# Kernel tuning notes

Hardware: AMD Instinct MI355X
Metric: run time of the kernel (lower is better)

Reference implementation:

```python
import jax, jax.numpy as jnp
import numpy as np

T, H, I, E, K, L, R = 1024, 2048, 1024, 16, 2, 4, 16


def setup_inputs() -> dict:
    key = jax.random.key(0)
    ks = jax.random.split(key, 10)
    hidden_states = jax.random.normal(ks[0], (T, H), jnp.float32)
    topk_ids = jax.random.randint(ks[1], (T, K), 0, E, dtype=jnp.int32)
    topk_weights = jax.random.uniform(ks[2], (T, K), jnp.float32)
    lora_indices = jax.random.randint(ks[3], (T,), 0, L, dtype=jnp.int32)
    lora_ranks = jax.random.randint(ks[4], (L,), 1, R + 1, dtype=jnp.int32)
    scalings = jax.random.uniform(ks[5], (L,), jnp.float32) + 0.5
    w1 = jax.random.normal(ks[6], (E, 2 * I, H), jnp.float32) * 0.02  # fused gate+up
    w2 = jax.random.normal(ks[7], (E, H, I), jnp.float32) * 0.02      # down proj
    lora_a = jax.random.normal(ks[8], (L, E, R, H), jnp.float32) * 0.02
    lora_b = jax.random.normal(ks[9], (L, E, H, R), jnp.float32) * 0.02
    return dict(hidden_states=hidden_states, topk_ids=topk_ids, topk_weights=topk_weights,
                lora_indices=lora_indices, lora_ranks=lora_ranks, scalings=scalings,
                w1=w1, w2=w2, lora_a=lora_a, lora_b=lora_b)


def reference(hidden_states, topk_ids, topk_weights, lora_indices, lora_ranks, scalings,
              w1, w2, lora_a, lora_b):
    x = hidden_states  # [T, H]
    # ---- Base FusedMoE (SiLU-gated), dense over all experts then routed ----
    h1 = jnp.einsum('th,efh->tef', x, w1)                 # [T, E, 2I]
    gate, up = jnp.split(h1, 2, axis=-1)                  # [T, E, I] each
    act = jax.nn.silu(gate) * up                          # [T, E, I]
    expert_out = jnp.einsum('tei,ehi->teh', act, w2)      # [T, E, H]
    route = jnp.zeros((T, E), x.dtype).at[jnp.arange(T)[:, None], topk_ids].add(topk_weights)
    base = jnp.einsum('te,teh->th', route, expert_out)    # [T, H]
    # ---- Per-expert LoRA delta (moe_dispatch + grouped LoRA GEMM) ----
    l_pair = jnp.broadcast_to(lora_indices[:, None], (T, K)).reshape(-1)  # [P], P=T*K
    e_pair = topk_ids.reshape(-1)                                         # [P]
    valid = l_pair >= 0
    l_safe = jnp.maximum(l_pair, 0)
    flat_idx = l_safe * E + e_pair                                        # index into [L*E, ...]
    A = jnp.take(lora_a.reshape(L * E, R, H), flat_idx, axis=0)           # [P, R, H]
    B = jnp.take(lora_b.reshape(L * E, H, R), flat_idx, axis=0)           # [P, H, R]
    xp = jnp.repeat(x, K, axis=0)                                         # [P, H]
    a = jnp.einsum('ph,prh->pr', xp, A)                                   # [P, R]
    ranks = jnp.maximum(lora_ranks, 1)
    rmask = jnp.arange(R)[None, :] < ranks[l_safe][:, None]               # variable rank mask
    a = jnp.where(rmask, a, 0.0) * scalings[l_safe][:, None]
    delta = jnp.einsum('pr,phr->ph', a, B)                                # [P, H]
    delta = jnp.where(valid[:, None], delta, 0.0)
    delta = delta.reshape(T, K, H).sum(axis=1)                            # merge (token,k) pairs
    return base + delta
```

## Files before the change

### kernel.cpp

```cpp
#include <hip/hip_runtime.h>
#include <math.h>

constexpr int T = 1024;
constexpr int H = 2048;
constexpr int I = 1024;
constexpr int E = 16;
constexpr int K = 2;
constexpr int L = 4;
constexpr int R = 16;
constexpr int P = T * K;
constexpr int MT_MAX = 48;
constexpr int G_CVT = T * H / (256 * 8);
constexpr int G1 = MT_MAX * 32;
constexpr int G2 = MT_MAX * 64;

typedef __attribute__((ext_vector_type(8))) short bf16x8;
typedef __attribute__((ext_vector_type(4))) float f32x4;

__device__ inline unsigned short f2bf(float f) {
  unsigned u = __builtin_bit_cast(unsigned, f);
  u = (u + 0x7FFFu + ((u >> 16) & 1u)) >> 16;
  return (unsigned short)u;
}

__device__ inline bf16x8 pack8(f32x4 a, f32x4 b) {
  bf16x8 v;
  v[0] = (short)f2bf(a[0]); v[1] = (short)f2bf(a[1]);
  v[2] = (short)f2bf(a[2]); v[3] = (short)f2bf(a[3]);
  v[4] = (short)f2bf(b[0]); v[5] = (short)f2bf(b[1]);
  v[6] = (short)f2bf(b[2]); v[7] = (short)f2bf(b[3]);
  return v;
}

__device__ inline void st8(unsigned short* s, int r, int c, bf16x8 v) {
  int byte = ((r << 6) + c) * 2;
  byte ^= (r & 7) << 4;
  *reinterpret_cast<bf16x8*>(reinterpret_cast<char*>(s) + byte) = v;
}
__device__ inline bf16x8 ld8(const unsigned short* s, int r, int c) {
  int byte = ((r << 6) + c) * 2;
  byte ^= (r & 7) << 4;
  return *reinterpret_cast<const bf16x8*>(reinterpret_cast<const char*>(s) + byte);
}

__global__ __launch_bounds__(256) void prep_kernel(
    const float* __restrict__ x, unsigned short* __restrict__ xb,
    float* __restrict__ out,
    const int* __restrict__ topk_ids, const float* __restrict__ topk_w,
    const int* __restrict__ lora_idx,
    int* __restrict__ eoff, int* __restrict__ pair_t,
    float* __restrict__ pair_w, int* __restrict__ pair_e,
    int* __restrict__ tile_e, int* __restrict__ tile_m0, int* __restrict__ ntiles) {
  const int tid = threadIdx.x;
  if (blockIdx.x < G_CVT) {
    const int i = (blockIdx.x * 256 + tid) * 8;
    f32x4 a = *reinterpret_cast<const f32x4*>(x + i);
    f32x4 b = *reinterpret_cast<const f32x4*>(x + i + 4);
    *reinterpret_cast<bf16x8*>(xb + i) = pack8(a, b);
    const f32x4 z = {0.f, 0.f, 0.f, 0.f};
    *reinterpret_cast<f32x4*>(out + i) = z;
    *reinterpret_cast<f32x4*>(out + i + 4) = z;
    return;
  }
  __shared__ int cnt2[E * L];
  __shared__ int off2[E * L + 1];
  __shared__ int cur2[E * L];
  if (tid < E * L) cnt2[tid] = 0;
  __syncthreads();
  for (int p = tid; p < P; p += 256) {
    const int e = topk_ids[p];
    int l = lora_idx[p / K];
    if (l < 0) l = 0;
    atomicAdd(&cnt2[e * L + l], 1);
  }
  __syncthreads();
  if (tid == 0) {
    off2[0] = 0;
    for (int b = 0; b < E * L; ++b) off2[b + 1] = off2[b] + cnt2[b];
    int nt = 0;
    for (int e = 0; e < E; ++e) {
      const int c = off2[(e + 1) * L] - off2[e * L];
      for (int m0 = 0; m0 < c; m0 += 64) {
        tile_e[nt] = e;
        tile_m0[nt] = m0;
        ++nt;
      }
    }
    *ntiles = nt;
  }
  __syncthreads();
  if (tid < E * L) cur2[tid] = off2[tid];
  if (tid <= E) eoff[tid] = off2[tid * L];
  __syncthreads();
  for (int p = tid; p < P; p += 256) {
    const int e = topk_ids[p];
    int l = lora_idx[p / K];
    if (l < 0) l = 0;
    const int pos = atomicAdd(&cur2[e * L + l], 1);
    pair_t[pos] = p / K;
    pair_w[pos] = topk_w[p];
    pair_e[pos] = e;
  }
}

__global__ __launch_bounds__(256) void gemm1_lora(
    const unsigned short* __restrict__ xb, const float* __restrict__ w1,
    const int* __restrict__ eoff, const int* __restrict__ pair_t,
    const int* __restrict__ tile_e, const int* __restrict__ tile_m0,
    const int* __restrict__ ntiles, unsigned short* __restrict__ act,
    const float* __restrict__ x, const float* __restrict__ lora_a,
    const float* __restrict__ lora_b, const int* __restrict__ lora_idx,
    const int* __restrict__ lora_ranks, const float* __restrict__ scalings,
    const int* __restrict__ pair_e, float* __restrict__ out) {
  __shared__ __align__(16) char smem[16384];
  const int tid = threadIdx.x;

  if (blockIdx.x < (unsigned)G1) {
    const int bid = blockIdx.x;
    const int mt = bid >> 5;
    if (mt >= *ntiles) return;
    const int it = bid & 31;
    const int e = tile_e[mt];
    const int m0 = tile_m0[mt];
    const int beg = eoff[e];
    const int cnt = eoff[e + 1] - beg;
    const int i0 = it * 32;

    unsigned short* sX = (unsigned short*)smem;
    unsigned short* sG = (unsigned short*)(smem + 8192);
    unsigned short* sU = (unsigned short*)(smem + 12288);

    const int xr = tid >> 2, xc = (tid & 3) * 16;
    const int gr = tid >> 3, gc = (tid & 7) * 8;

    const int rm = m0 + xr;
    const int tok = (rm < cnt) ? pair_t[beg + rm] : -1;
    const unsigned short* xrow = xb + (size_t)(tok < 0 ? 0 : tok) * H + xc;
    const float* grow = w1 + ((size_t)e * (2 * I) + i0 + gr) * H + gc;
    const float* urow = grow + (size_t)I * H;

    const int lane = tid & 63, wid = tid >> 6;
    const int wm = wid << 4;
    const int fr = lane & 15, fq = lane >> 4;

    f32x4 ag[2], au[2];
#pragma unroll
    for (int b = 0; b < 2; ++b) {
      ag[b] = {0.f, 0.f, 0.f, 0.f};
      au[b] = {0.f, 0.f, 0.f, 0.f};
    }

    bf16x8 rx[2];
    f32x4 rg[2], ru[2];
    const bf16x8 zero8 = {0, 0, 0, 0, 0, 0, 0, 0};

    auto LOAD = [&](int kk) {
      if (tok >= 0) {
        rx[0] = *reinterpret_cast<const bf16x8*>(xrow + kk);
        rx[1] = *reinterpret_cast<const bf16x8*>(xrow + kk + 8);
      } else {
        rx[0] = zero8; rx[1] = zero8;
      }
      rg[0] = *reinterpret_cast<const f32x4*>(grow + kk);
      rg[1] = *reinterpret_cast<const f32x4*>(grow + kk + 4);
      ru[0] = *reinterpret_cast<const f32x4*>(urow + kk);
      ru[1] = *reinterpret_cast<const f32x4*>(urow + kk + 4);
    };

    constexpr int NT = H / 64;
    LOAD(0);
    for (int t = 0; t < NT; ++t) {
      const bf16x8 wg = pack8(rg[0], rg[1]);
      const bf16x8 wu = pack8(ru[0], ru[1]);
      __syncthreads();
      st8(sX, xr, xc, rx[0]); st8(sX, xr, xc + 8, rx[1]);
      st8(sG, gr, gc, wg);
      st8(sU, gr, gc, wu);
      if (t + 1 < NT) LOAD((t + 1) * 64);
      __syncthreads();
#pragma unroll
      for (int kb = 0; kb < 2; ++kb) {
        const int k8 = (kb << 5) + (fq << 3);
        bf16x8 af = ld8(sX, wm + fr, k8);
        bf16x8 gf[2], uf[2];
#pragma unroll
        for (int nj = 0; nj < 2; ++nj) {
          gf[nj] = ld8(sG, (nj << 4) + fr, k8);
          uf[nj] = ld8(sU, (nj << 4) + fr, k8);
        }
#pragma unroll
        for (int nj = 0; nj < 2; ++nj) {
          ag[nj] = __builtin_amdgcn_mfma_f32_16x16x32_bf16(af, gf[nj], ag[nj], 0, 0, 0);
          au[nj] = __builtin_amdgcn_mfma_f32_16x16x32_bf16(af, uf[nj], au[nj], 0, 0, 0);
        }
      }
    }

#pragma unroll
    for (int q = 0; q < 4; ++q) {
      const int m = m0 + wm + (fq << 2) + q;
      if (m >= cnt) continue;
#pragma unroll
      for (int nj = 0; nj < 2; ++nj) {
        const float g = ag[nj][q];
        const float u = au[nj][q];
        const float s = g / (1.f + __expf(-g));
        act[(size_t)(beg + m) * I + i0 + (nj << 4) + fr] = f2bf(s * u);
      }
    }
    return;
  }

  const int p = blockIdx.x - G1;
  const int t = pair_t[p];
  const int e = pair_e[p];
  const int l = lora_idx[t];
  if (l < 0) return;
  int rank = lora_ranks[l];
  if (rank < 1) rank = 1;
  const float sc = scalings[l];

  float* a_sh = (float*)smem;
  const int wave = tid >> 6, lane = tid & 63;
  const float4* xv = reinterpret_cast<const float4*>(x + (size_t)t * H);
  const float* Ab = lora_a + (size_t)(l * E + e) * R * H;
#pragma unroll
  for (int q = 0; q < 4; ++q) {
    const int r = (wave << 2) | q;
    const float4* Av = reinterpret_cast<const float4*>(Ab + (size_t)r * H);
    float s = 0.f;
#pragma unroll
    for (int it2 = 0; it2 < H / 256; ++it2) {
      const int h4 = it2 * 64 + lane;
      const float4 xx = xv[h4];
      const float4 aa = Av[h4];
      s += xx.x * aa.x + xx.y * aa.y + xx.z * aa.z + xx.w * aa.w;
    }
#pragma unroll
    for (int off = 32; off; off >>= 1) s += __shfl_xor(s, off);
    if (lane == 0) a_sh[r] = (r < rank) ? s * sc : 0.f;
  }
  __syncthreads();
  const float* Bb = lora_b + (size_t)(l * E + e) * H * R;
  for (int h = tid; h < H; h += 256) {
    const float4* Bv = reinterpret_cast<const float4*>(Bb + (size_t)h * R);
    float d = 0.f;
#pragma unroll
    for (int r4 = 0; r4 < 4; ++r4) {
      const float4 bb = Bv[r4];
      d += a_sh[r4 * 4 + 0] * bb.x + a_sh[r4 * 4 + 1] * bb.y +
           a_sh[r4 * 4 + 2] * bb.z + a_sh[r4 * 4 + 3] * bb.w;
    }
    atomicAdd(out + (size_t)t * H + h, d);
  }
}

__global__ __launch_bounds__(256) void gemm2_mfma(
    const unsigned short* __restrict__ act, const float* __restrict__ w2,
    const int* __restrict__ eoff, const int* __restrict__ pair_t,
    const float* __restrict__ pair_w, const int* __restrict__ tile_e,
    const int* __restrict__ tile_m0, const int* __restrict__ ntiles,
    float* __restrict__ out) {
  const int bid = blockIdx.x;
  const int mt = bid >> 6;
  if (mt >= *ntiles) return;
  const int ht = bid & 63;
  const int e = tile_e[mt];
  const int m0 = tile_m0[mt];
  const int beg = eoff[e];
  const int cnt = eoff[e + 1] - beg;
  const int h0 = ht * 32;

  __shared__ unsigned short sA[64 * 64];
  __shared__ unsigned short sB[32 * 64];

  const int tid = threadIdx.x;
  const int ar = tid >> 2, ac = (tid & 3) * 16;
  const int br = tid >> 3, bc = (tid & 7) * 8;

  const bool av = (m0 + ar) < cnt;
  const unsigned short* arow = act + (size_t)(beg + (av ? m0 + ar : 0)) * I + ac;
  const float* brow = w2 + ((size_t)e * H + h0 + br) * I + bc;

  const int lane = tid & 63, wid = tid >> 6;
  const int wm = wid << 4;
  const int fr = lane & 15, fq = lane >> 4;

  f32x4 acc[2];
#pragma unroll
  for (int b = 0; b < 2; ++b) acc[b] = {0.f, 0.f, 0.f, 0.f};

  bf16x8 ra[2];
  f32x4 rb[2];

  auto LOAD = [&](int kk) {
    ra[0] = *reinterpret_cast<const bf16x8*>(arow + kk);
    ra[1] = *reinterpret_cast<const bf16x8*>(arow + kk + 8);
    rb[0] = *reinterpret_cast<const f32x4*>(brow + kk);
    rb[1] = *reinterpret_cast<const f32x4*>(brow + kk + 4);
  };

  constexpr int NT2 = I / 64;
  LOAD(0);
  for (int t = 0; t < NT2; ++t) {
    const bf16x8 wb = pack8(rb[0], rb[1]);
    __syncthreads();
    st8(sA, ar, ac, ra[0]); st8(sA, ar, ac + 8, ra[1]);
    st8(sB, br, bc, wb);
    if (t + 1 < NT2) LOAD((t + 1) * 64);
    __syncthreads();
#pragma unroll
    for (int kb = 0; kb < 2; ++kb) {
      const int k8 = (kb << 5) + (fq << 3);
      bf16x8 af = ld8(sA, wm + fr, k8);
      bf16x8 bf[2];
#pragma unroll
      for (int nj = 0; nj < 2; ++nj) bf[nj] = ld8(sB, (nj << 4) + fr, k8);
#pragma unroll
      for (int nj = 0; nj < 2; ++nj)
        acc[nj] = __builtin_amdgcn_mfma_f32_16x16x32_bf16(af, bf[nj], acc[nj], 0, 0, 0);
    }
  }

#pragma unroll
  for (int q = 0; q < 4; ++q) {
    const int m = m0 + wm + (fq << 2) + q;
    if (m >= cnt) continue;
    const int tt = pair_t[beg + m];
    const float w = pair_w[beg + m];
#pragma unroll
    for (int nj = 0; nj < 2; ++nj)
      atomicAdd(out + (size_t)tt * H + h0 + (nj << 4) + fr, w * acc[nj][q]);
  }
}

extern "C" void kernel_launch(void* const* d_in, const int* in_sizes, int n_in,
                              void* d_out, int out_size, void* d_ws, size_t ws_size,
                              hipStream_t stream) {
  const float* x          = (const float*)d_in[0];
  const int*   topk_ids   = (const int*)d_in[1];
  const float* topk_w     = (const float*)d_in[2];
  const int*   lora_idx   = (const int*)d_in[3];
  const int*   lora_ranks = (const int*)d_in[4];
  const float* scalings   = (const float*)d_in[5];
  const float* w1         = (const float*)d_in[6];
  const float* w2         = (const float*)d_in[7];
  const float* lora_a     = (const float*)d_in[8];
  const float* lora_b     = (const float*)d_in[9];
  float* out = (float*)d_out;

  char* ws = (char*)d_ws;
  int*   eoff    = (int*)(ws);
  int*   ntiles  = (int*)(ws + 96);
  int*   tile_e  = (int*)(ws + 256);
  int*   tile_m0 = (int*)(ws + 512);
  int*   pair_t  = (int*)(ws + 1024);
  int*   pair_e  = (int*)(ws + 1024 + 4 * P);
  float* pair_w  = (float*)(ws + 1024 + 8 * P);
  unsigned short* xb  = (unsigned short*)(ws + 32768);
  unsigned short* act = (unsigned short*)(ws + 32768 + (size_t)T * H * 2);

  prep_kernel<<<G_CVT + 1, 256, 0, stream>>>(x, xb, out, topk_ids, topk_w, lora_idx,
                                             eoff, pair_t, pair_w, pair_e, tile_e,
                                             tile_m0, ntiles);
  gemm1_lora<<<G1 + P, 256, 0, stream>>>(xb, w1, eoff, pair_t, tile_e, tile_m0, ntiles,
                                         act, x, lora_a, lora_b, lora_idx, lora_ranks,
                                         scalings, pair_e, out);
  gemm2_mfma<<<G2, 256, 0, stream>>>(act, w2, eoff, pair_t, pair_w, tile_e, tile_m0,
                                     ntiles, out);
}
```

Before: 187.2 us.

## Enlarge MoE GEMM M-tile to 128 rows with two-stage register prefetch

Both the gate/up GEMM and the down-projection GEMM now use 128-row token tiles instead of 64. Each wave computes a 2x2 grid of MFMA blocks, so every fp32 weight tile is loaded and converted to bf16 once per 128 rows instead of once per 64. The loop also alternates between two register buffers, so global loads are issued two k-steps ahead. The cost is more registers and LDS per block and fewer blocks (MT_MAX drops to 32), which can hurt occupancy and load balance across experts.

```diff
diff --git a/kernel.cpp b/kernel.cpp
--- a/kernel.cpp
+++ b/kernel.cpp
@@ -9,7 +9,7 @@
 constexpr int L = 4;
 constexpr int R = 16;
 constexpr int P = T * K;
-constexpr int MT_MAX = 48;
+constexpr int MT_MAX = 32;
 constexpr int G_CVT = T * H / (256 * 8);
 constexpr int G1 = MT_MAX * 32;
 constexpr int G2 = MT_MAX * 64;
@@ -80,7 +80,7 @@
     int nt = 0;
     for (int e = 0; e < E; ++e) {
       const int c = off2[(e + 1) * L] - off2[e * L];
-      for (int m0 = 0; m0 < c; m0 += 64) {
+      for (int m0 = 0; m0 < c; m0 += 128) {
         tile_e[nt] = e;
         tile_m0[nt] = m0;
         ++nt;
@@ -112,7 +112,7 @@
     const float* __restrict__ lora_b, const int* __restrict__ lora_idx,
     const int* __restrict__ lora_ranks, const float* __restrict__ scalings,
     const int* __restrict__ pair_e, float* __restrict__ out) {
-  __shared__ __align__(16) char smem[16384];
+  __shared__ __align__(16) char smem[24576];
   const int tid = threadIdx.x;
 
   if (blockIdx.x < (unsigned)G1) {
@@ -127,10 +127,10 @@
     const int i0 = it * 32;
 
     unsigned short* sX = (unsigned short*)smem;
-    unsigned short* sG = (unsigned short*)(smem + 8192);
-    unsigned short* sU = (unsigned short*)(smem + 12288);
-
-    const int xr = tid >> 2, xc = (tid & 3) * 16;
+    unsigned short* sG = (unsigned short*)(smem + 16384);
+    unsigned short* sU = (unsigned short*)(smem + 20480);
+
+    const int xr = tid >> 1, xc = (tid & 1) * 32;
     const int gr = tid >> 3, gc = (tid & 7) * 8;
 
     const int rm = m0 + xr;
@@ -140,74 +140,94 @@
     const float* urow = grow + (size_t)I * H;
 
     const int lane = tid & 63, wid = tid >> 6;
-    const int wm = wid << 4;
+    const int wm = wid << 5;
     const int fr = lane & 15, fq = lane >> 4;
 
-    f32x4 ag[2], au[2];
-#pragma unroll
-    for (int b = 0; b < 2; ++b) {
-      ag[b] = {0.f, 0.f, 0.f, 0.f};
-      au[b] = {0.f, 0.f, 0.f, 0.f};
+    f32x4 ag[2][2], au[2][2];
+#pragma unroll
+    for (int a = 0; a < 2; ++a)
+#pragma unroll
+      for (int b = 0; b < 2; ++b) {
+        ag[a][b] = {0.f, 0.f, 0.f, 0.f};
+        au[a][b] = {0.f, 0.f, 0.f, 0.f};
+      }
+
+    const bf16x8 zero8 = {0, 0, 0, 0, 0, 0, 0, 0};
+    bf16x8 rxA[4], rxB[4];
+    f32x4 rgA[2], ruA[2], rgB[2], ruB[2];
+
+#define G1_LOAD(RX, RG, RU, KK)                                             \
+    do {                                                                    \
+      if (tok >= 0) {                                                       \
+        RX[0] = *reinterpret_cast<const bf16x8*>(xrow + (KK));              \
+        RX[1] = *reinterpret_cast<const bf16x8*>(xrow + (KK) + 8);          \
+        RX[2] = *reinterpret_cast<const bf16x8*>(xrow + (KK) + 16);         \
+        RX[3] = *reinterpret_cast<const bf16x8*>(xrow + (KK) + 24);         \
+      } else {                                                              \
+        RX[0] = zero8; RX[1] = zero8; RX[2] = zero8; RX[3] = zero8;         \
+      }                                                                     \
+      RG[0] = *reinterpret_cast<const f32x4*>(grow + (KK));                 \
+      RG[1] = *reinterpret_cast<const f32x4*>(grow + (KK) + 4);             \
+      RU[0] = *reinterpret_cast<const f32x4*>(urow + (KK));                 \
+      RU[1] = *reinterpret_cast<const f32x4*>(urow + (KK) + 4);             \
+    } while (0)
+
+#define G1_STEP(RX, RG, RU, TNEXT, RXN, RGN, RUN)                           \
+    do {                                                                    \
+      const bf16x8 wg = pack8(RG[0], RG[1]);                                \
+      const bf16x8 wu = pack8(RU[0], RU[1]);                                \
+      __syncthreads();                                                      \
+      st8(sX, xr, xc, RX[0]); st8(sX, xr, xc + 8, RX[1]);                   \
+      st8(sX, xr, xc + 16, RX[2]); st8(sX, xr, xc + 24, RX[3]);             \
+      st8(sG, gr, gc, wg);                                                  \
+      st8(sU, gr, gc, wu);                                                  \
+      if ((TNEXT) < NT) G1_LOAD(RXN, RGN, RUN, (TNEXT) * 64);               \
+      __syncthreads();                                                      \
+      _Pragma("unroll")                                                     \
+      for (int kb = 0; kb < 2; ++kb) {                                      \
+        const int k8 = (kb << 5) + (fq << 3);                               \
+        bf16x8 af[2], gf[2], uf[2];                                         \
+        _Pragma("unroll")                                                   \
+        for (int mi = 0; mi < 2; ++mi) af[mi] = ld8(sX, wm + (mi << 4) + fr, k8); \
+        _Pragma("unroll")                                                   \
+        for (int nj = 0; nj < 2; ++nj) {                                    \
+          gf[nj] = ld8(sG, (nj << 4) + fr, k8);                             \
+          uf[nj] = ld8(sU, (nj << 4) + fr, k8);                             \
+        }                                                                   \
+        _Pragma("unroll")                                                   \
+        for (int mi = 0; mi < 2; ++mi)                                      \
+          _Pragma("unroll")                                                 \
+          for (int nj = 0; nj < 2; ++nj) {                                  \
+            ag[mi][nj] = __builtin_amdgcn_mfma_f32_16x16x32_bf16(af[mi], gf[nj], ag[mi][nj], 0, 0, 0); \
+            au[mi][nj] = __builtin_amdgcn_mfma_f32_16x16x32_bf16(af[mi], uf[nj], au[mi][nj], 0, 0, 0); \
+          }                                                                 \
+      }                                                                     \
+    } while (0)
+
+    constexpr int NT = H / 64;
+    G1_LOAD(rxA, rgA, ruA, 0);
+    G1_LOAD(rxB, rgB, ruB, 64);
+    for (int t = 0; t < NT; t += 2) {
+      G1_STEP(rxA, rgA, ruA, t + 2, rxA, rgA, ruA);
+      G1_STEP(rxB, rgB, ruB, t + 3, rxB, rgB, ruB);
     }
-
-    bf16x8 rx[2];
-    f32x4 rg[2], ru[2];
-    const bf16x8 zero8 = {0, 0, 0, 0, 0, 0, 0, 0};
-
-    auto LOAD = [&](int kk) {
-      if (tok >= 0) {
-        rx[0] = *reinterpret_cast<const bf16x8*>(xrow + kk);
-        rx[1] = *reinterpret_cast<const bf16x8*>(xrow + kk + 8);
-      } else {
-        rx[0] = zero8; rx[1] = zero8;
-      }
-      rg[0] = *reinterpret_cast<const f32x4*>(grow + kk);
-      rg[1] = *reinterpret_cast<const f32x4*>(grow + kk + 4);
-      ru[0] = *reinterpret_cast<const f32x4*>(urow + kk);
-      ru[1] = *reinterpret_cast<const f32x4*>(urow + kk + 4);
-    };
-
-    constexpr int NT = H / 64;
-    LOAD(0);
-    for (int t = 0; t < NT; ++t) {
-      const bf16x8 wg = pack8(rg[0], rg[1]);
-      const bf16x8 wu = pack8(ru[0], ru[1]);
-      __syncthreads();
-      st8(sX, xr, xc, rx[0]); st8(sX, xr, xc + 8, rx[1]);
-      st8(sG, gr, gc, wg);
-      st8(sU, gr, gc, wu);
-      if (t + 1 < NT) LOAD((t + 1) * 64);
-      __syncthreads();
-#pragma unroll
-      for (int kb = 0; kb < 2; ++kb) {
-        const int k8 = (kb << 5) + (fq << 3);
-        bf16x8 af = ld8(sX, wm + fr, k8);
-        bf16x8 gf[2], uf[2];
+#undef G1_LOAD
+#undef G1_STEP
+
+#pragma unroll
+    for (int mi = 0; mi < 2; ++mi)
+#pragma unroll
+      for (int q = 0; q < 4; ++q) {
+        const int m = m0 + wm + (mi << 4) + (fq << 2) + q;
+        if (m >= cnt) continue;
 #pragma unroll
         for (int nj = 0; nj < 2; ++nj) {
-          gf[nj] = ld8(sG, (nj << 4) + fr, k8);
-          uf[nj] = ld8(sU, (nj << 4) + fr, k8);
-        }
-#pragma unroll
-        for (int nj = 0; nj < 2; ++nj) {
-          ag[nj] = __builtin_amdgcn_mfma_f32_16x16x32_bf16(af, gf[nj], ag[nj], 0, 0, 0);
-          au[nj] = __builtin_amdgcn_mfma_f32_16x16x32_bf16(af, uf[nj], au[nj], 0, 0, 0);
+          const float g = ag[mi][nj][q];
+          const float u = au[mi][nj][q];
+          const float s = g / (1.f + __expf(-g));
+          act[(size_t)(beg + m) * I + i0 + (nj << 4) + fr] = f2bf(s * u);
         }
       }
-    }
-
-#pragma unroll
-    for (int q = 0; q < 4; ++q) {
-      const int m = m0 + wm + (fq << 2) + q;
-      if (m >= cnt) continue;
-#pragma unroll
-      for (int nj = 0; nj < 2; ++nj) {
-        const float g = ag[nj][q];
-        const float u = au[nj][q];
-        const float s = g / (1.f + __expf(-g));
-        act[(size_t)(beg + m) * I + i0 + (nj << 4) + fr] = f2bf(s * u);
-      }
-    }
     return;
   }
 
@@ -271,11 +291,11 @@
   const int cnt = eoff[e + 1] - beg;
   const int h0 = ht * 32;
 
-  __shared__ unsigned short sA[64 * 64];
+  __shared__ unsigned short sA[128 * 64];
   __shared__ unsigned short sB[32 * 64];
 
   const int tid = threadIdx.x;
-  const int ar = tid >> 2, ac = (tid & 3) * 16;
+  const int ar = tid >> 1, ac = (tid & 1) * 32;
   const int br = tid >> 3, bc = (tid & 7) * 8;
 
   const bool av = (m0 + ar) < cnt;
@@ -283,55 +303,75 @@
   const float* brow = w2 + ((size_t)e * H + h0 + br) * I + bc;
 
   const int lane = tid & 63, wid = tid >> 6;
-  const int wm = wid << 4;
+  const int wm = wid << 5;
   const int fr = lane & 15, fq = lane >> 4;
 
-  f32x4 acc[2];
-#pragma unroll
-  for (int b = 0; b < 2; ++b) acc[b] = {0.f, 0.f, 0.f, 0.f};
-
-  bf16x8 ra[2];
-  f32x4 rb[2];
-
-  auto LOAD = [&](int kk) {
-    ra[0] = *reinterpret_cast<const bf16x8*>(arow + kk);
-    ra[1] = *reinterpret_cast<const bf16x8*>(arow + kk + 8);
-    rb[0] = *reinterpret_cast<const f32x4*>(brow + kk);
-    rb[1] = *reinterpret_cast<const f32x4*>(brow + kk + 4);
-  };
+  f32x4 acc[2][2];
+#pragma unroll
+  for (int a = 0; a < 2; ++a)
+#pragma unroll
+    for (int b = 0; b < 2; ++b) acc[a][b] = {0.f, 0.f, 0.f, 0.f};
+
+  bf16x8 raA[4], raB[4];
+  f32x4 rbA[2], rbB[2];
+
+#define G2_LOAD(RA, RB, KK)                                                 \
+  do {                                                                      \
+    RA[0] = *reinterpret_cast<const bf16x8*>(arow + (KK));                  \
+    RA[1] = *reinterpret_cast<const bf16x8*>(arow + (KK) + 8);              \
+    RA[2] = *reinterpret_cast<const bf16x8*>(arow + (KK) + 16);             \
+    RA[3] = *reinterpret_cast<const bf16x8*>(arow + (KK) + 24);             \
+    RB[0] = *reinterpret_cast<const f32x4*>(brow + (KK));                   \
+    RB[1] = *reinterpret_cast<const f32x4*>(brow + (KK) + 4);               \
+  } while (0)
+
+#define G2_STEP(RA, RB, TNEXT, RAN, RBN)                                    \
+  do {                                                                      \
+    const bf16x8 wb = pack8(RB[0], RB[1]);                                  \
+    __syncthreads();                                                        \
+    st8(sA, ar, ac, RA[0]); st8(sA, ar, ac + 8, RA[1]);                     \
+    st8(sA, ar, ac + 16, RA[2]); st8(sA, ar, ac + 24, RA[3]);               \
+    st8(sB, br, bc, wb);                                                    \
+    if ((TNEXT) < NT2) G2_LOAD(RAN, RBN, (TNEXT) * 64);                     \
+    __syncthreads();                                                        \
+    _Pragma("unroll")                                                       \
+    for (int kb = 0; kb < 2; ++kb) {                                        \
+      const int k8 = (kb << 5) + (fq << 3);                                 \
+      bf16x8 af[2], bf[2];                                                  \
+      _Pragma("unroll")                                                     \
+      for (int mi = 0; mi < 2; ++mi) af[mi] = ld8(sA, wm + (mi << 4) + fr, k8); \
+      _Pragma("unroll")                                                     \
+      for (int nj = 0; nj < 2; ++nj) bf[nj] = ld8(sB, (nj << 4) + fr, k8);  \
+      _Pragma("unroll")                                                     \
+      for (int mi = 0; mi < 2; ++mi)                                        \
+        _Pragma("unroll")                                                   \
+        for (int nj = 0; nj < 2; ++nj)                                      \
+          acc[mi][nj] = __builtin_amdgcn_mfma_f32_16x16x32_bf16(af[mi], bf[nj], acc[mi][nj], 0, 0, 0); \
+    }                                                                       \
+  } while (0)
 
   constexpr int NT2 = I / 64;
-  LOAD(0);
-  for (int t = 0; t < NT2; ++t) {
-    const bf16x8 wb = pack8(rb[0], rb[1]);
-    __syncthreads();
-    st8(sA, ar, ac, ra[0]); st8(sA, ar, ac + 8, ra[1]);
-    st8(sB, br, bc, wb);
-    if (t + 1 < NT2) LOAD((t + 1) * 64);
-    __syncthreads();
-#pragma unroll
-    for (int kb = 0; kb < 2; ++kb) {
-      const int k8 = (kb << 5) + (fq << 3);
-      bf16x8 af = ld8(sA, wm + fr, k8);
-      bf16x8 bf[2];
-#pragma unroll
-      for (int nj = 0; nj < 2; ++nj) bf[nj] = ld8(sB, (nj << 4) + fr, k8);
+  G2_LOAD(raA, rbA, 0);
+  G2_LOAD(raB, rbB, 64);
+  for (int t = 0; t < NT2; t += 2) {
+    G2_STEP(raA, rbA, t + 2, raA, rbA);
+    G2_STEP(raB, rbB, t + 3, raB, rbB);
+  }
+#undef G2_LOAD
+#undef G2_STEP
+
+#pragma unroll
+  for (int mi = 0; mi < 2; ++mi)
+#pragma unroll
+    for (int q = 0; q < 4; ++q) {
+      const int m = m0 + wm + (mi << 4) + (fq << 2) + q;
+      if (m >= cnt) continue;
+      const int tt = pair_t[beg + m];
+      const float w = pair_w[beg + m];
 #pragma unroll
       for (int nj = 0; nj < 2; ++nj)
-        acc[nj] = __builtin_amdgcn_mfma_f32_16x16x32_bf16(af, bf[nj], acc[nj], 0, 0, 0);
+        atomicAdd(out + (size_t)tt * H + h0 + (nj << 4) + fr, w * acc[mi][nj][q]);
     }
-  }
-
-#pragma unroll
-  for (int q = 0; q < 4; ++q) {
-    const int m = m0 + wm + (fq << 2) + q;
-    if (m >= cnt) continue;
-    const int tt = pair_t[beg + m];
-    const float w = pair_w[beg + m];
-#pragma unroll
-    for (int nj = 0; nj < 2; ++nj)
-      atomicAdd(out + (size_t)tt * H + h0 + (nj << 4) + fr, w * acc[nj][q]);
-  }
 }
 
 extern "C" void kernel_launch(void* const* d_in, const int* in_sizes, int n_in,
```

Measured after the change: 191.8 us. 2.4% more time.

## Drop LDS staging in grouped MoE GEMMs and load MFMA fragments directly

Applied to the files above, without the earlier changes.

Both expert GEMMs now skip shared memory and the per-step barriers: each wave reads its bf16 activation rows and fp32 weight rows straight from global memory into MFMA operand registers. Row tiles grow from 64 to 128 pairs, each wave computes a 32-row slab, and the gemm1 column tile shrinks from 32 to 16, so the number of M tiles and the grid layout change. This removes LDS traffic and synchronisation but loses cross-wave reuse of loaded weights, so global and cache traffic per FLOP rises. Weights are still converted to bf16 per load.

```diff
diff --git a/kernel.cpp b/kernel.cpp
--- a/kernel.cpp
+++ b/kernel.cpp
@@ -9,9 +9,9 @@
 constexpr int L = 4;
 constexpr int R = 16;
 constexpr int P = T * K;
-constexpr int MT_MAX = 48;
+constexpr int MT_MAX = 32;
 constexpr int G_CVT = T * H / (256 * 8);
-constexpr int G1 = MT_MAX * 32;
+constexpr int G1 = MT_MAX * 64;
 constexpr int G2 = MT_MAX * 64;
 
 typedef __attribute__((ext_vector_type(8))) short bf16x8;
@@ -30,17 +30,6 @@
   v[4] = (short)f2bf(b[0]); v[5] = (short)f2bf(b[1]);
   v[6] = (short)f2bf(b[2]); v[7] = (short)f2bf(b[3]);
   return v;
-}
-
-__device__ inline void st8(unsigned short* s, int r, int c, bf16x8 v) {
-  int byte = ((r << 6) + c) * 2;
-  byte ^= (r & 7) << 4;
-  *reinterpret_cast<bf16x8*>(reinterpret_cast<char*>(s) + byte) = v;
-}
-__device__ inline bf16x8 ld8(const unsigned short* s, int r, int c) {
-  int byte = ((r << 6) + c) * 2;
-  byte ^= (r & 7) << 4;
-  return *reinterpret_cast<const bf16x8*>(reinterpret_cast<const char*>(s) + byte);
 }
 
 __global__ __launch_bounds__(256) void prep_kernel(
@@ -80,7 +69,7 @@
     int nt = 0;
     for (int e = 0; e < E; ++e) {
       const int c = off2[(e + 1) * L] - off2[e * L];
-      for (int m0 = 0; m0 < c; m0 += 64) {
+      for (int m0 = 0; m0 < c; m0 += 128) {
         tile_e[nt] = e;
         tile_m0[nt] = m0;
         ++nt;
@@ -112,100 +101,68 @@
     const float* __restrict__ lora_b, const int* __restrict__ lora_idx,
     const int* __restrict__ lora_ranks, const float* __restrict__ scalings,
     const int* __restrict__ pair_e, float* __restrict__ out) {
-  __shared__ __align__(16) char smem[16384];
+  __shared__ float a_sh[R];
   const int tid = threadIdx.x;
 
   if (blockIdx.x < (unsigned)G1) {
     const int bid = blockIdx.x;
-    const int mt = bid >> 5;
+    const int mt = bid >> 6;
     if (mt >= *ntiles) return;
-    const int it = bid & 31;
+    const int it = bid & 63;
     const int e = tile_e[mt];
     const int m0 = tile_m0[mt];
     const int beg = eoff[e];
     const int cnt = eoff[e + 1] - beg;
-    const int i0 = it * 32;
-
-    unsigned short* sX = (unsigned short*)smem;
-    unsigned short* sG = (unsigned short*)(smem + 8192);
-    unsigned short* sU = (unsigned short*)(smem + 12288);
-
-    const int xr = tid >> 2, xc = (tid & 3) * 16;
-    const int gr = tid >> 3, gc = (tid & 7) * 8;
-
-    const int rm = m0 + xr;
-    const int tok = (rm < cnt) ? pair_t[beg + rm] : -1;
-    const unsigned short* xrow = xb + (size_t)(tok < 0 ? 0 : tok) * H + xc;
-    const float* grow = w1 + ((size_t)e * (2 * I) + i0 + gr) * H + gc;
-    const float* urow = grow + (size_t)I * H;
+    const int i0 = it * 16;
 
     const int lane = tid & 63, wid = tid >> 6;
-    const int wm = wid << 4;
+    const int wm = wid << 5;
     const int fr = lane & 15, fq = lane >> 4;
 
-    f32x4 ag[2], au[2];
-#pragma unroll
-    for (int b = 0; b < 2; ++b) {
-      ag[b] = {0.f, 0.f, 0.f, 0.f};
-      au[b] = {0.f, 0.f, 0.f, 0.f};
-    }
-
-    bf16x8 rx[2];
-    f32x4 rg[2], ru[2];
-    const bf16x8 zero8 = {0, 0, 0, 0, 0, 0, 0, 0};
-
-    auto LOAD = [&](int kk) {
-      if (tok >= 0) {
-        rx[0] = *reinterpret_cast<const bf16x8*>(xrow + kk);
-        rx[1] = *reinterpret_cast<const bf16x8*>(xrow + kk + 8);
-      } else {
-        rx[0] = zero8; rx[1] = zero8;
+    const int mr0 = m0 + wm + fr;
+    const int mr1 = mr0 + 16;
+    const int t0 = pair_t[beg + (mr0 < cnt ? mr0 : 0)];
+    const int t1 = pair_t[beg + (mr1 < cnt ? mr1 : 0)];
+    const unsigned short* xr0 = xb + (size_t)t0 * H + (fq << 3);
+    const unsigned short* xr1 = xb + (size_t)t1 * H + (fq << 3);
+    const float* gw = w1 + ((size_t)e * (2 * I) + i0 + fr) * H + (fq << 3);
+    const float* uw = gw + (size_t)I * H;
+
+    f32x4 ag0 = {0.f, 0.f, 0.f, 0.f}, ag1 = {0.f, 0.f, 0.f, 0.f};
+    f32x4 au0 = {0.f, 0.f, 0.f, 0.f}, au1 = {0.f, 0.f, 0.f, 0.f};
+
+    for (int kk = 0; kk < H; kk += 64) {
+#pragma unroll
+      for (int kb = 0; kb < 2; ++kb) {
+        const int off = kk + (kb << 5);
+        const bf16x8 a0 = *reinterpret_cast<const bf16x8*>(xr0 + off);
+        const bf16x8 a1 = *reinterpret_cast<const bf16x8*>(xr1 + off);
+        const f32x4 g0 = *reinterpret_cast<const f32x4*>(gw + off);
+        const f32x4 g1 = *reinterpret_cast<const f32x4*>(gw + off + 4);
+        const f32x4 u0 = *reinterpret_cast<const f32x4*>(uw + off);
+        const f32x4 u1 = *reinterpret_cast<const f32x4*>(uw + off + 4);
+        const bf16x8 gf = pack8(g0, g1);
+        const bf16x8 uf = pack8(u0, u1);
+        ag0 = __builtin_amdgcn_mfma_f32_16x16x32_bf16(a0, gf, ag0, 0, 0, 0);
+        au0 = __builtin_amdgcn_mfma_f32_16x16x32_bf16(a0, uf, au0, 0, 0, 0);
+        ag1 = __builtin_amdgcn_mfma_f32_16x16x32_bf16(a1, gf, ag1, 0, 0, 0);
+        au1 = __builtin_amdgcn_mfma_f32_16x16x32_bf16(a1, uf, au1, 0, 0, 0);
       }
-      rg[0] = *reinterpret_cast<const f32x4*>(grow + kk);
-      rg[1] = *reinterpret_cast<const f32x4*>(grow + kk + 4);
-      ru[0] = *reinterpret_cast<const f32x4*>(urow + kk);
-      ru[1] = *reinterpret_cast<const f32x4*>(urow + kk + 4);
-    };
-
-    constexpr int NT = H / 64;
-    LOAD(0);
-    for (int t = 0; t < NT; ++t) {
-      const bf16x8 wg = pack8(rg[0], rg[1]);
-      const bf16x8 wu = pack8(ru[0], ru[1]);
-      __syncthreads();
-      st8(sX, xr, xc, rx[0]); st8(sX, xr, xc + 8, rx[1]);
-      st8(sG, gr, gc, wg);
-      st8(sU, gr, gc, wu);
-      if (t + 1 < NT) LOAD((t + 1) * 64);
-      __syncthreads();
-#pragma unroll
-      for (int kb = 0; kb < 2; ++kb) {
-        const int k8 = (kb << 5) + (fq << 3);
-        bf16x8 af = ld8(sX, wm + fr, k8);
-        bf16x8 gf[2], uf[2];
-#pragma unroll
-        for (int nj = 0; nj < 2; ++nj) {
-          gf[nj] = ld8(sG, (nj << 4) + fr, k8);
-          uf[nj] = ld8(sU, (nj << 4) + fr, k8);
-        }
-#pragma unroll
-        for (int nj = 0; nj < 2; ++nj) {
-          ag[nj] = __builtin_amdgcn_mfma_f32_16x16x32_bf16(af, gf[nj], ag[nj], 0, 0, 0);
-          au[nj] = __builtin_amdgcn_mfma_f32_16x16x32_bf16(af, uf[nj], au[nj], 0, 0, 0);
-        }
+    }
+
+#pragma unroll
+    for (int q = 0; q < 4; ++q) {
+      const int m_0 = m0 + wm + (fq << 2) + q;
+      if (m_0 < cnt) {
+        const float g = ag0[q];
+        const float s = g / (1.f + __expf(-g));
+        act[(size_t)(beg + m_0) * I + i0 + fr] = f2bf(s * au0[q]);
       }
-    }
-
-#pragma unroll
-    for (int q = 0; q < 4; ++q) {
-      const int m = m0 + wm + (fq << 2) + q;
-      if (m >= cnt) continue;
-#pragma unroll
-      for (int nj = 0; nj < 2; ++nj) {
-        const float g = ag[nj][q];
-        const float u = au[nj][q];
+      const int m_1 = m_0 + 16;
+      if (m_1 < cnt) {
+        const float g = ag1[q];
         const float s = g / (1.f + __expf(-g));
-        act[(size_t)(beg + m) * I + i0 + (nj << 4) + fr] = f2bf(s * u);
+        act[(size_t)(beg + m_1) * I + i0 + fr] = f2bf(s * au1[q]);
       }
     }
     return;
@@ -220,7 +177,6 @@
   if (rank < 1) rank = 1;
   const float sc = scalings[l];
 
-  float* a_sh = (float*)smem;
   const int wave = tid >> 6, lane = tid & 63;
   const float4* xv = reinterpret_cast<const float4*>(x + (size_t)t * H);
   const float* Ab = lora_a + (size_t)(l * E + e) * R * H;
@@ -271,66 +227,58 @@
   const int cnt = eoff[e + 1] - beg;
   const int h0 = ht * 32;
 
-  __shared__ unsigned short sA[64 * 64];
-  __shared__ unsigned short sB[32 * 64];
-
   const int tid = threadIdx.x;
-  const int ar = tid >> 2, ac = (tid & 3) * 16;
-  const int br = tid >> 3, bc = (tid & 7) * 8;
-
-  const bool av = (m0 + ar) < cnt;
-  const unsigned short* arow = act + (size_t)(beg + (av ? m0 + ar : 0)) * I + ac;
-  const float* brow = w2 + ((size_t)e * H + h0 + br) * I + bc;
-
   const int lane = tid & 63, wid = tid >> 6;
-  const int wm = wid << 4;
+  const int wm = wid << 5;
   const int fr = lane & 15, fq = lane >> 4;
 
-  f32x4 acc[2];
-#pragma unroll
-  for (int b = 0; b < 2; ++b) acc[b] = {0.f, 0.f, 0.f, 0.f};
-
-  bf16x8 ra[2];
-  f32x4 rb[2];
-
-  auto LOAD = [&](int kk) {
-    ra[0] = *reinterpret_cast<const bf16x8*>(arow + kk);
-    ra[1] = *reinterpret_cast<const bf16x8*>(arow + kk + 8);
-    rb[0] = *reinterpret_cast<const f32x4*>(brow + kk);
-    rb[1] = *reinterpret_cast<const f32x4*>(brow + kk + 4);
-  };
-
-  constexpr int NT2 = I / 64;
-  LOAD(0);
-  for (int t = 0; t < NT2; ++t) {
-    const bf16x8 wb = pack8(rb[0], rb[1]);
-    __syncthreads();
-    st8(sA, ar, ac, ra[0]); st8(sA, ar, ac + 8, ra[1]);
-    st8(sB, br, bc, wb);
-    if (t + 1 < NT2) LOAD((t + 1) * 64);
-    __syncthreads();
+  const int mr0 = m0 + wm + fr;
+  const int mr1 = mr0 + 16;
+  const unsigned short* ar0 =
+      act + (size_t)(beg + (mr0 < cnt ? mr0 : 0)) * I + (fq << 3);
+  const unsigned short* ar1 =
+      act + (size_t)(beg + (mr1 < cnt ? mr1 : 0)) * I + (fq << 3);
+  const float* br0 = w2 + ((size_t)e * H + h0 + fr) * I + (fq << 3);
+  const float* br1 = br0 + (size_t)16 * I;
+
+  f32x4 acc00 = {0.f, 0.f, 0.f, 0.f}, acc01 = {0.f, 0.f, 0.f, 0.f};
+  f32x4 acc10 = {0.f, 0.f, 0.f, 0.f}, acc11 = {0.f, 0.f, 0.f, 0.f};
+
+  for (int kk = 0; kk < I; kk += 64) {
 #pragma unroll
     for (int kb = 0; kb < 2; ++kb) {
-      const int k8 = (kb << 5) + (fq << 3);
-      bf16x8 af = ld8(sA, wm + fr, k8);
-      bf16x8 bf[2];
-#pragma unroll
-      for (int nj = 0; nj < 2; ++nj) bf[nj] = ld8(sB, (nj << 4) + fr, k8);
-#pragma unroll
-      for (int nj = 0; nj < 2; ++nj)
-        acc[nj] = __builtin_amdgcn_mfma_f32_16x16x32_bf16(af, bf[nj], acc[nj], 0, 0, 0);
+      const int off = kk + (kb << 5);
+      const bf16x8 a0 = *reinterpret_cast<const bf16x8*>(ar0 + off);
+      const bf16x8 a1 = *reinterpret_cast<const bf16x8*>(ar1 + off);
+      const f32x4 b00 = *reinterpret_cast<const f32x4*>(br0 + off);
+      const f32x4 b01 = *reinterpret_cast<const f32x4*>(br0 + off + 4);
+      const f32x4 b10 = *reinterpret_cast<const f32x4*>(br1 + off);
+      const f32x4 b11 = *reinterpret_cast<const f32x4*>(br1 + off + 4);
+      const bf16x8 bf0 = pack8(b00, b01);
+      const bf16x8 bf1 = pack8(b10, b11);
+      acc00 = __builtin_amdgcn_mfma_f32_16x16x32_bf16(a0, bf0, acc00, 0, 0, 0);
+      acc01 = __builtin_amdgcn_mfma_f32_16x16x32_bf16(a0, bf1, acc01, 0, 0, 0);
+      acc10 = __builtin_amdgcn_mfma_f32_16x16x32_bf16(a1, bf0, acc10, 0, 0, 0);
+      acc11 = __builtin_amdgcn_mfma_f32_16x16x32_bf16(a1, bf1, acc11, 0, 0, 0);
     }
   }
 
 #pragma unroll
   for (int q = 0; q < 4; ++q) {
-    const int m = m0 + wm + (fq << 2) + q;
-    if (m >= cnt) continue;
-    const int tt = pair_t[beg + m];
-    const float w = pair_w[beg + m];
-#pragma unroll
-    for (int nj = 0; nj < 2; ++nj)
-      atomicAdd(out + (size_t)tt * H + h0 + (nj << 4) + fr, w * acc[nj][q]);
+    const int m_0 = m0 + wm + (fq << 2) + q;
+    if (m_0 < cnt) {
+      const int tt = pair_t[beg + m_0];
+      const float w = pair_w[beg + m_0];
+      atomicAdd(out + (size_t)tt * H + h0 + fr, w * acc00[q]);
+      atomicAdd(out + (size_t)tt * H + h0 + 16 + fr, w * acc01[q]);
+    }
+    const int m_1 = m_0 + 16;
+    if (m_1 < cnt) {
+      const int tt = pair_t[beg + m_1];
+      const float w = pair_w[beg + m_1];
+      atomicAdd(out + (size_t)tt * H + h0 + fr, w * acc10[q]);
+      atomicAdd(out + (size_t)tt * H + h0 + 16 + fr, w * acc11[q]);
+    }
   }
 }
 
```

Result: slower. 416.0 us (+122.3%).
